# Kernel tuning notes

Measured on AMD Instinct MI355X. Metric: run time of the kernel, lower is better.

The kernel has to match this reference:

```python
import jax, jax.numpy as jnp
import numpy as np

C_IN, H, T_OUT, C_OUT = 16, 256, 24, 8


def setup_inputs() -> dict:
    key = jax.random.key(0)
    ks = jax.random.split(key, 8)
    s_ih = 1.0 / np.sqrt(H)
    x = jax.random.normal(ks[0], (8192, C_IN, 48), dtype=jnp.float32)
    # Encoder LSTMCell params (PyTorch layout: gates stacked [i, f, g, o], each H rows)
    enc_Wih = jax.random.uniform(ks[1], (4 * H, C_IN), minval=-s_ih, maxval=s_ih, dtype=jnp.float32)
    enc_Whh = jax.random.uniform(ks[2], (4 * H, H), minval=-s_ih, maxval=s_ih, dtype=jnp.float32)
    enc_b = jax.random.uniform(ks[3], (4 * H,), minval=-s_ih, maxval=s_ih, dtype=jnp.float32)  # b_ih + b_hh folded
    # Decoder LSTMCell has input_size=0 -> W_ih is (4H, 0), contributes nothing
    dec_Whh = jax.random.uniform(ks[4], (4 * H, H), minval=-s_ih, maxval=s_ih, dtype=jnp.float32)
    dec_b = jax.random.uniform(ks[5], (4 * H,), minval=-s_ih, maxval=s_ih, dtype=jnp.float32)
    # TimestepDense: per-timestep (non-shared) linear H -> C_OUT, dropout inactive at eval
    dense_W = jax.random.uniform(ks[6], (T_OUT, C_OUT, H), minval=-s_ih, maxval=s_ih, dtype=jnp.float32)
    dense_b = jax.random.uniform(ks[7], (T_OUT, C_OUT), minval=-s_ih, maxval=s_ih, dtype=jnp.float32)
    return {"x": x, "enc_Wih": enc_Wih, "enc_Whh": enc_Whh, "enc_b": enc_b,
            "dec_Whh": dec_Whh, "dec_b": dec_b, "dense_W": dense_W, "dense_b": dense_b}


def _lstm_step(h, c, gates):
    i, f, g, o = jnp.split(gates, 4, axis=-1)
    c_new = jax.nn.sigmoid(f) * c + jax.nn.sigmoid(i) * jnp.tanh(g)
    h_new = jax.nn.sigmoid(o) * jnp.tanh(c_new)
    return h_new, c_new


def reference(x, enc_Wih, enc_Whh, enc_b, dec_Whh, dec_b, dense_W, dense_b):
    N = x.shape[0]
    # ----- Encoder: scan over T input steps -----
    xt = jnp.transpose(x, (2, 0, 1))  # (T, N, C)
    h0 = jnp.zeros((N, H), dtype=x.dtype)
    c0 = jnp.zeros((N, H), dtype=x.dtype)

    def enc_step(carry, x_t):
        h, c = carry
        gates = x_t @ enc_Wih.T + h @ enc_Whh.T + enc_b  # (N, 4H)
        h, c = _lstm_step(h, c, gates)
        return (h, c), None

    (h_enc, _), _ = jax.lax.scan(enc_step, (h0, c0), xt)

    # ----- Decoder: zero-input LSTM cell, collect hidden states -----
    def dec_step(carry, _):
        h, c = carry
        gates = h @ dec_Whh.T + dec_b
        h, c = _lstm_step(h, c, gates)
        return (h, c), h

    (_, _), hs = jax.lax.scan(dec_step, (h_enc, c0), None, length=T_OUT)  # hs: (T_OUT, N, H)

    # ----- TimestepDense: per-timestep linear H -> C_OUT (eval mode, dropout off) -----
    out = jnp.einsum('tnh,toh->not', hs, dense_W) + dense_b.T[None]  # (N, C_OUT, T_OUT)
    return out
```

## Files before the change

kernel.cpp:

```cpp
#include <hip/hip_runtime.h>

typedef __attribute__((ext_vector_type(8))) _Float16 f16x8;
typedef __attribute__((ext_vector_type(4))) float    f32x4;

#define HD    256
#define CIN   16
#define TIN   48
#define TOUT  24
#define COUT  8
#define MB    32
#define KPAD  296
#define KT_ENC 9
#define KT_DEC 8
#define WE_HALVES (KT_ENC*4*16*512)
#define WD_HALVES (KT_DEC*4*16*512)
#define PREP_TOTAL (WE_HALVES + WD_HALVES)

template <int N> struct KTag { static constexpr int val = N; };

__global__ void prep_frags(const float* __restrict__ enc_Wih,
                           const float* __restrict__ enc_Whh,
                           const float* __restrict__ dec_Whh,
                           _Float16* __restrict__ wf)
{
    int p = blockIdx.x * blockDim.x + threadIdx.x;
    if (p >= PREP_TOTAL) return;
    int lane = (p >> 3) & 63;
    int s    = p & 7;
    int kq   = ((lane >> 4) << 3) + s;
    int l15  = lane & 15;
    float v;
    if (p < WE_HALVES) {
        int frag = p >> 9;
        int kt = frag >> 6, g = (frag >> 4) & 3, ntile = frag & 15;
        int k   = kt * 32 + kq;
        int row = g * 256 + ntile * 16 + l15;
        v = 0.0f;
        if (k < 256)      v = enc_Whh[row * 256 + k];
        else if (k < 272) v = enc_Wih[row * 16 + (k - 256)];
    } else {
        int q = p - WE_HALVES;
        int frag = q >> 9;
        int kt = frag >> 6, g = (frag >> 4) & 3, ntile = frag & 15;
        int k   = kt * 32 + kq;
        int row = g * 256 + ntile * 16 + l15;
        v = dec_Whh[row * 256 + k];
    }
    wf[p] = (_Float16)v;
}

__device__ __forceinline__ float sigm(float v) {
    return __builtin_amdgcn_rcpf(1.0f + __expf(-v));
}
__device__ __forceinline__ float tanh_f(float v) {
    return 1.0f - 2.0f * __builtin_amdgcn_rcpf(1.0f + __expf(2.0f * v));
}

__device__ __forceinline__ void gld_lds16(const _Float16* g, _Float16* l) {
    __builtin_amdgcn_global_load_lds(
        (const __attribute__((address_space(1))) void*)g,
        (__attribute__((address_space(3))) void*)l, 16, 0, 0);
}

__global__ __launch_bounds__(1024, 1) void seq2seq_mfma(
    const float* __restrict__ x,
    const _Float16* __restrict__ wf,
    const float* __restrict__ enc_b,
    const float* __restrict__ dec_b,
    const float* __restrict__ denseW,
    const float* __restrict__ denseb,
    float* __restrict__ out)
{
    __shared__ __align__(16) _Float16 hF[MB * KPAD];
    __shared__ __align__(16) _Float16 Wlds[16][2][4][512];
    __shared__ __align__(16) float    outS4[MB * COUT * 4];

    const int tid  = threadIdx.x;
    const int w    = tid >> 6;
    const int lane = tid & 63;
    const int quad = lane >> 4;
    const int l15  = lane & 15;
    const int n0   = blockIdx.x * MB;

    float bE[4], bD[4];
    #pragma unroll
    for (int g = 0; g < 4; ++g) {
        int col = w * 16 + l15;
        bE[g] = enc_b[g * 256 + col];
        bD[g] = dec_b[g * 256 + col];
    }

    for (int i = tid; i < MB * KPAD; i += 1024) hF[i] = (_Float16)0.0f;
    __syncthreads();
    if (tid < 512) {
        int m = tid >> 4, c = tid & 15;
        hF[m * KPAD + 256 + c] = (_Float16)x[(size_t)(n0 + m) * (CIN * TIN) + c * TIN];
    }
    __syncthreads();

    f32x4 acc[2][4];
    float cst[2][4];
    #pragma unroll
    for (int mt = 0; mt < 2; ++mt)
        #pragma unroll
        for (int r = 0; r < 4; ++r) cst[mt][r] = 0.0f;

    const f16x8* Ap0 = (const f16x8*)(hF + l15 * KPAD);
    const f16x8* Ap1 = (const f16x8*)(hF + (16 + l15) * KPAD);

    auto stage = [&](int buf, int kt, const _Float16* __restrict__ Wbase) {
        #pragma unroll
        for (int g = 0; g < 4; ++g) {
            const _Float16* gp = Wbase + (size_t)(kt * 64 + g * 16 + w) * 512 + lane * 8;
            gld_lds16(gp, &Wlds[w][buf][g][0]);
        }
    };

    auto gemm = [&](auto kt_tag, const _Float16* __restrict__ Wbase, const float (&bias)[4]) {
        constexpr int KT = decltype(kt_tag)::val;
        #pragma unroll
        for (int mt = 0; mt < 2; ++mt)
            #pragma unroll
            for (int g = 0; g < 4; ++g) {
                float b = bias[g];
                f32x4 bv = {b, b, b, b};
                acc[mt][g] = bv;
            }
        stage(0, 0, Wbase);
        #pragma unroll
        for (int kt = 0; kt < KT; ++kt) {
            if (kt + 1 < KT) {
                stage((kt + 1) & 1, kt + 1, Wbase);
                asm volatile("s_waitcnt vmcnt(4)" ::: "memory");
            } else {
                asm volatile("s_waitcnt vmcnt(0)" ::: "memory");
            }
            __builtin_amdgcn_sched_barrier(0);
            f16x8 a0 = Ap0[kt * 4 + quad];
            f16x8 a1 = Ap1[kt * 4 + quad];
            const int b = kt & 1;
            #pragma unroll
            for (int g = 0; g < 4; ++g) {
                f16x8 bf = *(const f16x8*)&Wlds[w][b][g][lane * 8];
                acc[0][g] = __builtin_amdgcn_mfma_f32_16x16x32_f16(a0, bf, acc[0][g], 0, 0, 0);
                acc[1][g] = __builtin_amdgcn_mfma_f32_16x16x32_f16(a1, bf, acc[1][g], 0, 0, 0);
            }
        }
    };

    auto pointwise = [&]() {
        int col = w * 16 + l15;
        #pragma unroll
        for (int mt = 0; mt < 2; ++mt)
            #pragma unroll
            for (int r = 0; r < 4; ++r) {
                float iv = sigm(acc[mt][0][r]);
                float fv = sigm(acc[mt][1][r]);
                float gv = tanh_f(acc[mt][2][r]);
                float ov = sigm(acc[mt][3][r]);
                float cn = fmaf(fv, cst[mt][r], iv * gv);
                cst[mt][r] = cn;
                float hv = ov * tanh_f(cn);
                hF[(mt * 16 + quad * 4 + r) * KPAD + col] = (_Float16)hv;
            }
    };

    for (int t = 0; t < TIN; ++t) {
        float xv = 0.0f;
        const bool xl = (tid < 512) && (t + 1 < TIN);
        if (xl)
            xv = x[(size_t)(n0 + (tid >> 4)) * (CIN * TIN) + (tid & 15) * TIN + (t + 1)];
        gemm(KTag<KT_ENC>{}, wf, bE);
        __syncthreads();
        pointwise();
        if (xl) hF[(tid >> 4) * KPAD + 256 + (tid & 15)] = (_Float16)xv;
        __syncthreads();
    }

    #pragma unroll
    for (int mt = 0; mt < 2; ++mt)
        #pragma unroll
        for (int r = 0; r < 4; ++r) cst[mt][r] = 0.0f;

    for (int t = 0; t < TOUT; ++t) {
        gemm(KTag<KT_DEC>{}, wf + WE_HALVES, bD);
        __syncthreads();
        pointwise();
        __syncthreads();
        if (tid < MB * COUT) {
            int m = tid >> 3, o = tid & 7;
            const float* wr = denseW + (t * COUT + o) * HD;
            float s = denseb[t * COUT + o];
            #pragma unroll 4
            for (int j8 = 0; j8 < 32; ++j8) {
                f16x8 hv  = *(const f16x8*)(hF + m * KPAD + j8 * 8);
                float4 w0 = *(const float4*)(wr + j8 * 8);
                float4 w1 = *(const float4*)(wr + j8 * 8 + 4);
                s = fmaf((float)hv[0], w0.x, s);
                s = fmaf((float)hv[1], w0.y, s);
                s = fmaf((float)hv[2], w0.z, s);
                s = fmaf((float)hv[3], w0.w, s);
                s = fmaf((float)hv[4], w1.x, s);
                s = fmaf((float)hv[5], w1.y, s);
                s = fmaf((float)hv[6], w1.z, s);
                s = fmaf((float)hv[7], w1.w, s);
            }
            outS4[(tid << 2) | (t & 3)] = s;
            if ((t & 3) == 3) {
                float4 v = *(const float4*)&outS4[tid << 2];
                *(float4*)(out + (size_t)(n0 + m) * (COUT * TOUT) + o * TOUT + (t - 3)) = v;
            }
        }
    }
}

extern "C" void kernel_launch(void* const* d_in, const int* in_sizes, int n_in,
                              void* d_out, int out_size, void* d_ws, size_t ws_size,
                              hipStream_t stream) {
    const float* x       = (const float*)d_in[0];
    const float* enc_Wih = (const float*)d_in[1];
    const float* enc_Whh = (const float*)d_in[2];
    const float* enc_b   = (const float*)d_in[3];
    const float* dec_Whh = (const float*)d_in[4];
    const float* dec_b   = (const float*)d_in[5];
    const float* denseW  = (const float*)d_in[6];
    const float* denseb  = (const float*)d_in[7];
    float* out = (float*)d_out;
    _Float16* wf = (_Float16*)d_ws;

    prep_frags<<<(PREP_TOTAL + 255) / 256, 256, 0, stream>>>(enc_Wih, enc_Whh, dec_Whh, wf);
    seq2seq_mfma<<<8192 / MB, 1024, 0, stream>>>(x, wf, enc_b, dec_b, denseW, denseb, out);
}
```

Before: 1.139 ms.

## Deepen weight staging pipeline to per-fragment ring of eight LDS slots

Replaces the per-k-tile double buffer (four fragments per stage) with an eight-slot ring of single fragments, keeping seven global-to-LDS loads in flight and waiting per fragment. It aims to hide global/L2 latency of the weight stream better inside the recurrent GEMM. The finer waitcnt granularity adds more sync points, and there is no barrier guarding slot reuse. Each wave only reads its own slots, so this depends on per-wave ordering.

```diff
diff --git a/kernel.cpp b/kernel.cpp
--- a/kernel.cpp
+++ b/kernel.cpp
@@ -72,7 +72,7 @@
     float* __restrict__ out)
 {
     __shared__ __align__(16) _Float16 hF[MB * KPAD];
-    __shared__ __align__(16) _Float16 Wlds[16][2][4][512];
+    __shared__ __align__(16) _Float16 Wlds[16][8][512];
     __shared__ __align__(16) float    outS4[MB * COUT * 4];
 
     const int tid  = threadIdx.x;
@@ -108,16 +108,15 @@
     const f16x8* Ap0 = (const f16x8*)(hF + l15 * KPAD);
     const f16x8* Ap1 = (const f16x8*)(hF + (16 + l15) * KPAD);
 
-    auto stage = [&](int buf, int kt, const _Float16* __restrict__ Wbase) {
-        #pragma unroll
-        for (int g = 0; g < 4; ++g) {
-            const _Float16* gp = Wbase + (size_t)(kt * 64 + g * 16 + w) * 512 + lane * 8;
-            gld_lds16(gp, &Wlds[w][buf][g][0]);
-        }
+    auto stagef = [&](int f, const _Float16* __restrict__ Wbase) {
+        int kt = f >> 2, g = f & 3;
+        const _Float16* gp = Wbase + (size_t)(kt * 64 + g * 16 + w) * 512 + lane * 8;
+        gld_lds16(gp, &Wlds[w][f & 7][0]);
     };
 
     auto gemm = [&](auto kt_tag, const _Float16* __restrict__ Wbase, const float (&bias)[4]) {
         constexpr int KT = decltype(kt_tag)::val;
+        constexpr int NF = KT * 4;
         #pragma unroll
         for (int mt = 0; mt < 2; ++mt)
             #pragma unroll
@@ -126,26 +125,33 @@
                 f32x4 bv = {b, b, b, b};
                 acc[mt][g] = bv;
             }
-        stage(0, 0, Wbase);
-        #pragma unroll
-        for (int kt = 0; kt < KT; ++kt) {
-            if (kt + 1 < KT) {
-                stage((kt + 1) & 1, kt + 1, Wbase);
-                asm volatile("s_waitcnt vmcnt(4)" ::: "memory");
-            } else {
-                asm volatile("s_waitcnt vmcnt(0)" ::: "memory");
-            }
+        f16x8 a0, a1;
+        auto body = [&](int f) {
+            int kt = f >> 2, g = f & 3;
+            if ((f & 3) == 0) {
+                a0 = Ap0[kt * 4 + quad];
+                a1 = Ap1[kt * 4 + quad];
+            }
+            f16x8 bf = *(const f16x8*)&Wlds[w][f & 7][lane * 8];
+            acc[0][g] = __builtin_amdgcn_mfma_f32_16x16x32_f16(a0, bf, acc[0][g], 0, 0, 0);
+            acc[1][g] = __builtin_amdgcn_mfma_f32_16x16x32_f16(a1, bf, acc[1][g], 0, 0, 0);
+        };
+        #pragma unroll
+        for (int f = 0; f < 7; ++f) stagef(f, Wbase);
+        #pragma unroll
+        for (int f = 0; f < NF - 7; ++f) {
+            stagef(f + 7, Wbase);
+            asm volatile("s_waitcnt vmcnt(7)" ::: "memory");
             __builtin_amdgcn_sched_barrier(0);
-            f16x8 a0 = Ap0[kt * 4 + quad];
-            f16x8 a1 = Ap1[kt * 4 + quad];
-            const int b = kt & 1;
-            #pragma unroll
-            for (int g = 0; g < 4; ++g) {
-                f16x8 bf = *(const f16x8*)&Wlds[w][b][g][lane * 8];
-                acc[0][g] = __builtin_amdgcn_mfma_f32_16x16x32_f16(a0, bf, acc[0][g], 0, 0, 0);
-                acc[1][g] = __builtin_amdgcn_mfma_f32_16x16x32_f16(a1, bf, acc[1][g], 0, 0, 0);
-            }
+            body(f);
         }
+        asm volatile("s_waitcnt vmcnt(6)" ::: "memory"); __builtin_amdgcn_sched_barrier(0); body(NF - 7);
+        asm volatile("s_waitcnt vmcnt(5)" ::: "memory"); __builtin_amdgcn_sched_barrier(0); body(NF - 6);
+        asm volatile("s_waitcnt vmcnt(4)" ::: "memory"); __builtin_amdgcn_sched_barrier(0); body(NF - 5);
+        asm volatile("s_waitcnt vmcnt(3)" ::: "memory"); __builtin_amdgcn_sched_barrier(0); body(NF - 4);
+        asm volatile("s_waitcnt vmcnt(2)" ::: "memory"); __builtin_amdgcn_sched_barrier(0); body(NF - 3);
+        asm volatile("s_waitcnt vmcnt(1)" ::: "memory"); __builtin_amdgcn_sched_barrier(0); body(NF - 2);
+        asm volatile("s_waitcnt vmcnt(0)" ::: "memory"); __builtin_amdgcn_sched_barrier(0); body(NF - 1);
     };
 
     auto pointwise = [&]() {
```

Measured after the change: 1.125 ms (median of 3 runs). Within noise of the previous version (-1.2%).

## Double-buffer hidden state and stream weight fragments through a 7-slot LDS ring

Applied to the files above, without the earlier changes.

Hidden state is double-buffered in LDS so each step reads h from one buffer and writes the new h to the other, which removes one of the two block barriers per timestep. Weight staging changes from per-kt double buffering (4 fragments, waitcnt 4) to a per-fragment ring of 7 slots that keeps 6 loads in flight and prefetches the next step's first fragments across step boundaries. The goal is to hide global/L2 weight-fetch latency behind MFMAs and cut synchronisation stalls. The cost is extra LDS for the second h buffer, plus a rolling slot index that has to stay consistent across the encoder/decoder transition.

```diff
diff --git a/kernel.cpp b/kernel.cpp
--- a/kernel.cpp
+++ b/kernel.cpp
@@ -12,6 +12,7 @@
 #define KPAD  296
 #define KT_ENC 9
 #define KT_DEC 8
+#define NSLOT 7
 #define WE_HALVES (KT_ENC*4*16*512)
 #define WD_HALVES (KT_DEC*4*16*512)
 #define PREP_TOTAL (WE_HALVES + WD_HALVES)
@@ -71,8 +72,8 @@
     const float* __restrict__ denseb,
     float* __restrict__ out)
 {
-    __shared__ __align__(16) _Float16 hF[MB * KPAD];
-    __shared__ __align__(16) _Float16 Wlds[16][2][4][512];
+    __shared__ __align__(16) _Float16 hF[2][MB * KPAD];
+    __shared__ __align__(16) _Float16 Wlds[16][NSLOT][512];
     __shared__ __align__(16) float    outS4[MB * COUT * 4];
 
     const int tid  = threadIdx.x;
@@ -90,11 +91,14 @@
         bD[g] = dec_b[g * 256 + col];
     }
 
-    for (int i = tid; i < MB * KPAD; i += 1024) hF[i] = (_Float16)0.0f;
+    {
+        _Float16* hz = &hF[0][0];
+        for (int i = tid; i < 2 * MB * KPAD; i += 1024) hz[i] = (_Float16)0.0f;
+    }
     __syncthreads();
     if (tid < 512) {
         int m = tid >> 4, c = tid & 15;
-        hF[m * KPAD + 256 + c] = (_Float16)x[(size_t)(n0 + m) * (CIN * TIN) + c * TIN];
+        hF[0][m * KPAD + 256 + c] = (_Float16)x[(size_t)(n0 + m) * (CIN * TIN) + c * TIN];
     }
     __syncthreads();
 
@@ -105,19 +109,21 @@
         #pragma unroll
         for (int r = 0; r < 4; ++r) cst[mt][r] = 0.0f;
 
-    const f16x8* Ap0 = (const f16x8*)(hF + l15 * KPAD);
-    const f16x8* Ap1 = (const f16x8*)(hF + (16 + l15) * KPAD);
-
-    auto stage = [&](int buf, int kt, const _Float16* __restrict__ Wbase) {
-        #pragma unroll
-        for (int g = 0; g < 4; ++g) {
-            const _Float16* gp = Wbase + (size_t)(kt * 64 + g * 16 + w) * 512 + lane * 8;
-            gld_lds16(gp, &Wlds[w][buf][g][0]);
-        }
+    auto fragptr = [&](const _Float16* __restrict__ Wbase, int f) {
+        int kt = f >> 2, g = f & 3;
+        return Wbase + (size_t)(kt * 64 + g * 16 + w) * 512 + lane * 8;
     };
 
-    auto gemm = [&](auto kt_tag, const _Float16* __restrict__ Wbase, const float (&bias)[4]) {
+    int rs = 0;
+    #pragma unroll
+    for (int f = 0; f < 6; ++f)
+        gld_lds16(fragptr(wf, f), &Wlds[w][f][0]);
+
+    auto gemm = [&](auto kt_tag, const _Float16* __restrict__ Wcur,
+                    const _Float16* __restrict__ Wnext,
+                    const float (&bias)[4], const _Float16* __restrict__ hR) {
         constexpr int KT = decltype(kt_tag)::val;
+        constexpr int NF = KT * 4;
         #pragma unroll
         for (int mt = 0; mt < 2; ++mt)
             #pragma unroll
@@ -126,29 +132,33 @@
                 f32x4 bv = {b, b, b, b};
                 acc[mt][g] = bv;
             }
-        stage(0, 0, Wbase);
-        #pragma unroll
-        for (int kt = 0; kt < KT; ++kt) {
-            if (kt + 1 < KT) {
-                stage((kt + 1) & 1, kt + 1, Wbase);
-                asm volatile("s_waitcnt vmcnt(4)" ::: "memory");
-            } else {
-                asm volatile("s_waitcnt vmcnt(0)" ::: "memory");
-            }
+        const f16x8* Ap0 = (const f16x8*)(hR + l15 * KPAD);
+        const f16x8* Ap1 = (const f16x8*)(hR + (16 + l15) * KPAD);
+        f16x8 a0, a1;
+        #pragma unroll
+        for (int f = 0; f < NF; ++f) {
+            {
+                const _Float16* gp = (f + 6 < NF) ? fragptr(Wcur, f + 6)
+                                                  : fragptr(Wnext, f + 6 - NF);
+                int ss = rs + 6; if (ss >= NSLOT) ss -= NSLOT;
+                gld_lds16(gp, &Wlds[w][ss][0]);
+            }
+            asm volatile("s_waitcnt vmcnt(6)" ::: "memory");
             __builtin_amdgcn_sched_barrier(0);
-            f16x8 a0 = Ap0[kt * 4 + quad];
-            f16x8 a1 = Ap1[kt * 4 + quad];
-            const int b = kt & 1;
-            #pragma unroll
-            for (int g = 0; g < 4; ++g) {
-                f16x8 bf = *(const f16x8*)&Wlds[w][b][g][lane * 8];
-                acc[0][g] = __builtin_amdgcn_mfma_f32_16x16x32_f16(a0, bf, acc[0][g], 0, 0, 0);
-                acc[1][g] = __builtin_amdgcn_mfma_f32_16x16x32_f16(a1, bf, acc[1][g], 0, 0, 0);
-            }
+            if ((f & 3) == 0) {
+                a0 = Ap0[(f >> 2) * 4 + quad];
+                a1 = Ap1[(f >> 2) * 4 + quad];
+            }
+            f16x8 bf = *(const f16x8*)&Wlds[w][rs][lane * 8];
+            constexpr int gg0 = 0;  (void)gg0;
+            const int g = f & 3;
+            acc[0][g] = __builtin_amdgcn_mfma_f32_16x16x32_f16(a0, bf, acc[0][g], 0, 0, 0);
+            acc[1][g] = __builtin_amdgcn_mfma_f32_16x16x32_f16(a1, bf, acc[1][g], 0, 0, 0);
+            rs = (rs + 1 == NSLOT) ? 0 : rs + 1;
         }
     };
 
-    auto pointwise = [&]() {
+    auto pointwise = [&](_Float16* __restrict__ hW) {
         int col = w * 16 + l15;
         #pragma unroll
         for (int mt = 0; mt < 2; ++mt)
@@ -161,20 +171,21 @@
                 float cn = fmaf(fv, cst[mt][r], iv * gv);
                 cst[mt][r] = cn;
                 float hv = ov * tanh_f(cn);
-                hF[(mt * 16 + quad * 4 + r) * KPAD + col] = (_Float16)hv;
+                hW[(mt * 16 + quad * 4 + r) * KPAD + col] = (_Float16)hv;
             }
     };
 
+    const _Float16* wfD = wf + WE_HALVES;
+
     for (int t = 0; t < TIN; ++t) {
+        gemm(KTag<KT_ENC>{}, wf, (t + 1 < TIN) ? wf : wfD, bE, hF[t & 1]);
         float xv = 0.0f;
         const bool xl = (tid < 512) && (t + 1 < TIN);
         if (xl)
             xv = x[(size_t)(n0 + (tid >> 4)) * (CIN * TIN) + (tid & 15) * TIN + (t + 1)];
-        gemm(KTag<KT_ENC>{}, wf, bE);
+        pointwise(hF[(t + 1) & 1]);
+        if (xl) hF[(t + 1) & 1][(tid >> 4) * KPAD + 256 + (tid & 15)] = (_Float16)xv;
         __syncthreads();
-        pointwise();
-        if (xl) hF[(tid >> 4) * KPAD + 256 + (tid & 15)] = (_Float16)xv;
-        __syncthreads();
     }
 
     #pragma unroll
@@ -183,17 +194,17 @@
         for (int r = 0; r < 4; ++r) cst[mt][r] = 0.0f;
 
     for (int t = 0; t < TOUT; ++t) {
-        gemm(KTag<KT_DEC>{}, wf + WE_HALVES, bD);
-        __syncthreads();
-        pointwise();
+        gemm(KTag<KT_DEC>{}, wfD, wfD, bD, hF[t & 1]);
+        pointwise(hF[(t + 1) & 1]);
         __syncthreads();
         if (tid < MB * COUT) {
             int m = tid >> 3, o = tid & 7;
             const float* wr = denseW + (t * COUT + o) * HD;
             float s = denseb[t * COUT + o];
+            const _Float16* hrow = &hF[(t + 1) & 1][m * KPAD];
             #pragma unroll 4
             for (int j8 = 0; j8 < 32; ++j8) {
-                f16x8 hv  = *(const f16x8*)(hF + m * KPAD + j8 * 8);
+                f16x8 hv  = *(const f16x8*)(hrow + j8 * 8);
                 float4 w0 = *(const float4*)(wr + j8 * 8);
                 float4 w1 = *(const float4*)(wr + j8 * 8 + 4);
                 s = fmaf((float)hv[0], w0.x, s);
```

After: 1.503 ms. 31.9% more time.
